# Performance work log

Hardware: AMD Instinct MI355X
Metric: run time of the kernel (lower is better)

Reference implementation:

```python
import jax, jax.numpy as jnp
import numpy as np

BZ, SEQ, IN_SZ, HID_SZ = 256, 512, 256, 256


def setup_inputs() -> dict:
    key = jax.random.key(0)
    k1, k2, k3, k4, k5 = jax.random.split(key, 5)
    stdv = 1.0 / np.sqrt(HID_SZ)
    return {
        "encoder_inputs": jax.random.normal(k1, (BZ, HID_SZ), dtype=jnp.float32),
        "decoder_inputs": jax.random.normal(k2, (BZ, SEQ, IN_SZ), dtype=jnp.float32),
        "U_i": jax.random.uniform(k3, (IN_SZ, HID_SZ), minval=-stdv, maxval=stdv, dtype=jnp.float32),
        "V_i": jax.random.uniform(k4, (HID_SZ, HID_SZ), minval=-stdv, maxval=stdv, dtype=jnp.float32),
        "b_i": jax.random.uniform(k5, (HID_SZ,), minval=-stdv, maxval=stdv, dtype=jnp.float32),
    }


def reference(encoder_inputs, decoder_inputs, U_i, V_i, b_i):
    # Sequential vanilla-RNN recurrence over time via lax.scan.
    # h_t = tanh(x_t @ U_i + h_{t-1} @ V_i + b_i)
    xs = jnp.swapaxes(decoder_inputs, 0, 1)  # [seq, bz, in]

    def step(h, x_t):
        h_new = jnp.tanh(x_t @ U_i + h @ V_i + b_i)
        return h_new, h_new

    _, outs = jax.lax.scan(step, encoder_inputs, xs)  # outs: [seq, bz, hid]
    decoder_outputs = jnp.swapaxes(outs, 0, 1)  # [bz, seq, hid]
    return (encoder_inputs, decoder_outputs)
```

## Files before the change

### kernel.cpp

```cpp
#include <hip/hip_runtime.h>
#include <hip/hip_bf16.h>


#define SEQn   512
#define HIDn   256
#define CHUNK  64
#define NCHUNK 8

typedef __attribute__((ext_vector_type(4))) float    floatx4;
typedef __attribute__((ext_vector_type(8))) _Float16 half8;

#define LDS_BARRIER() asm volatile("s_waitcnt lgkmcnt(0)\n\ts_barrier" ::: "memory")

__global__ __launch_bounds__(512, 1)
void rnn_fused(const float* __restrict__ enc, const float* __restrict__ x,
               const float* __restrict__ U,   const float* __restrict__ V,
               const float* __restrict__ bias, float* __restrict__ out)
{
    __shared__ _Float16 xbf[CHUNK][HIDn];
    __shared__ float    xu[CHUNK][HIDn + 1];
    __shared__ _Float16 hbuf[2][HIDn];

    const int tid = threadIdx.x;
    const int w   = tid >> 6;
    const int l   = tid & 63;
    const int lr  = l & 15;
    const int q   = l >> 4;
    const int b   = blockIdx.x;
    const int c0  = 32 * w + lr;

    half8 uf[2][8], vf[2][8];
    #pragma unroll
    for (int c = 0; c < 8; c++) {
        const float* up = U + (size_t)(32 * c + 8 * q) * HIDn + c0;
        const float* vp = V + (size_t)(32 * c + 8 * q) * HIDn + c0;
        #pragma unroll
        for (int nt = 0; nt < 2; nt++) {
            half8 tu, tv;
            #pragma unroll
            for (int j = 0; j < 8; j++) {
                tu[j] = (_Float16)up[(size_t)j * HIDn + 16 * nt];
                tv[j] = (_Float16)vp[(size_t)j * HIDn + 16 * nt];
            }
            uf[nt][c] = tu;
            vf[nt][c] = tv;
        }
    }

    const float b0 = bias[c0];
    const float b1 = bias[c0 + 16];

    if (tid < HIDn) {
        float h0 = enc[(size_t)b * HIDn + tid];
        out[(size_t)b * HIDn + tid] = h0;
        hbuf[0][tid] = (_Float16)h0;
    }

    const float* xb = x + (size_t)b * SEQn * HIDn;
    float* outDec   = out + (size_t)65536 + (size_t)b * SEQn * HIDn;

    const int srow = tid >> 3;
    const int scol = (tid & 7) * 32;

    const floatx4 zf = {0.f, 0.f, 0.f, 0.f};

    int p = 0;
    for (int g = 0; g < NCHUNK; g++) {
        const float* xs = xb + (size_t)(g * CHUNK + srow) * HIDn + scol;
        float4 xv[8];
        #pragma unroll
        for (int i = 0; i < 8; i++)
            xv[i] = *(const float4*)(xs + 4 * i);
        #pragma unroll
        for (int gi = 0; gi < 4; gi++) {
            half8 t;
            t[0] = (_Float16)xv[2*gi].x;   t[1] = (_Float16)xv[2*gi].y;
            t[2] = (_Float16)xv[2*gi].z;   t[3] = (_Float16)xv[2*gi].w;
            t[4] = (_Float16)xv[2*gi+1].x; t[5] = (_Float16)xv[2*gi+1].y;
            t[6] = (_Float16)xv[2*gi+1].z; t[7] = (_Float16)xv[2*gi+1].w;
            int grp = ((tid & 7) * 4 + gi) ^ (srow & 7);
            *(half8*)&xbf[srow][grp * 8] = t;
        }
        LDS_BARRIER();

        {
            floatx4 ga[2][4];
            #pragma unroll
            for (int c = 0; c < 8; c++) {
                half8 am[4];
                #pragma unroll
                for (int mt = 0; mt < 4; mt++) {
                    int row = 16 * mt + lr;
                    int grp = (4 * c + q) ^ (row & 7);
                    am[mt] = *(const half8*)&xbf[row][grp * 8];
                }
                #pragma unroll
                for (int mt = 0; mt < 4; mt++) {
                    ga[0][mt] = __builtin_amdgcn_mfma_f32_16x16x32_f16(
                        am[mt], uf[0][c], c ? ga[0][mt] : zf, 0, 0, 0);
                    ga[1][mt] = __builtin_amdgcn_mfma_f32_16x16x32_f16(
                        am[mt], uf[1][c], c ? ga[1][mt] : zf, 0, 0, 0);
                }
            }
            #pragma unroll
            for (int mt = 0; mt < 4; mt++)
                #pragma unroll
                for (int r = 0; r < 4; r++) {
                    int row = 16 * mt + 4 * q + r;
                    xu[row][c0]      = ga[0][mt][r] + b0;
                    xu[row][c0 + 16] = ga[1][mt][r] + b1;
                }
        }
        LDS_BARRIER();

        for (int tt = 0; tt < CHUNK; tt++) {
            half8 af[8];
            #pragma unroll
            for (int c = 0; c < 8; c++)
                af[c] = *(const half8*)&hbuf[p][32 * c + 8 * q];

            floatx4 acc[2][4];
            #pragma unroll
            for (int c = 0; c < 8; c++) {
                acc[0][c & 3] = __builtin_amdgcn_mfma_f32_16x16x32_f16(
                    af[c], vf[0][c], (c < 4) ? zf : acc[0][c & 3], 0, 0, 0);
                acc[1][c & 3] = __builtin_amdgcn_mfma_f32_16x16x32_f16(
                    af[c], vf[1][c], (c < 4) ? zf : acc[1][c & 3], 0, 0, 0);
            }

            float s0 = ((acc[0][0][0] + acc[0][1][0]) + (acc[0][2][0] + acc[0][3][0]))
                       + xu[tt][c0];
            float s1 = ((acc[1][0][0] + acc[1][1][0]) + (acc[1][2][0] + acc[1][3][0]))
                       + xu[tt][c0 + 16];
            float e0  = __expf(2.f * s0);
            float e1  = __expf(2.f * s1);
            float hv0 = 1.f - __fdividef(2.f, e0 + 1.f);
            float hv1 = 1.f - __fdividef(2.f, e1 + 1.f);

            if (q == 0) {
                hbuf[p ^ 1][c0]      = (_Float16)hv0;
                hbuf[p ^ 1][c0 + 16] = (_Float16)hv1;
                float* op = outDec + (size_t)(g * CHUNK + tt) * HIDn;
                op[c0]      = hv0;
                op[c0 + 16] = hv1;
            }
            p ^= 1;
            LDS_BARRIER();
        }
    }
}

extern "C" void kernel_launch(void* const* d_in, const int* in_sizes, int n_in,
                              void* d_out, int out_size, void* d_ws, size_t ws_size,
                              hipStream_t stream) {
    const float* enc  = (const float*)d_in[0];
    const float* x    = (const float*)d_in[1];
    const float* U    = (const float*)d_in[2];
    const float* V    = (const float*)d_in[3];
    const float* bias = (const float*)d_in[4];
    float* out = (float*)d_out;

    rnn_fused<<<256, 512, 0, stream>>>(enc, x, U, V, bias, out);
}
```

Before: 486.2 us.

## Halve block to four waves, each wave computing 64 hidden columns

The block shrinks from 8 waves to 4, and each wave now owns 64 hidden columns (four 16-wide MFMA tiles) instead of 32. In the recurrence, all 64 lanes now compute one tanh each and write the new h directly. Before, only the first quarter of each wave did this work. The aim is a cheaper per-timestep barrier and fuller lane use on the serial path. The cost is one wave per SIMD carrying twice the MFMA chain per step, with less latency hiding and higher register pressure from the doubled U/V fragments.

```diff
diff --git a/kernel.cpp b/kernel.cpp
--- a/kernel.cpp
+++ b/kernel.cpp
@@ -8,11 +8,12 @@
 #define NCHUNK 8
 
 typedef __attribute__((ext_vector_type(4))) float    floatx4;
+typedef __attribute__((ext_vector_type(4))) _Float16 half4;
 typedef __attribute__((ext_vector_type(8))) _Float16 half8;
 
 #define LDS_BARRIER() asm volatile("s_waitcnt lgkmcnt(0)\n\ts_barrier" ::: "memory")
 
-__global__ __launch_bounds__(512, 1)
+__global__ __launch_bounds__(256, 1)
 void rnn_fused(const float* __restrict__ enc, const float* __restrict__ x,
                const float* __restrict__ U,   const float* __restrict__ V,
                const float* __restrict__ bias, float* __restrict__ out)
@@ -27,15 +28,15 @@
     const int lr  = l & 15;
     const int q   = l >> 4;
     const int b   = blockIdx.x;
-    const int c0  = 32 * w + lr;
+    const int cw  = 64 * w;
 
-    half8 uf[2][8], vf[2][8];
+    half8 uf[4][8], vf[4][8];
     #pragma unroll
     for (int c = 0; c < 8; c++) {
-        const float* up = U + (size_t)(32 * c + 8 * q) * HIDn + c0;
-        const float* vp = V + (size_t)(32 * c + 8 * q) * HIDn + c0;
+        const float* up = U + (size_t)(32 * c + 8 * q) * HIDn + cw + lr;
+        const float* vp = V + (size_t)(32 * c + 8 * q) * HIDn + cw + lr;
         #pragma unroll
-        for (int nt = 0; nt < 2; nt++) {
+        for (int nt = 0; nt < 4; nt++) {
             half8 tu, tv;
             #pragma unroll
             for (int j = 0; j < 8; j++) {
@@ -47,10 +48,11 @@
         }
     }
 
-    const float b0 = bias[c0];
-    const float b1 = bias[c0 + 16];
+    float bv[4];
+    #pragma unroll
+    for (int nt = 0; nt < 4; nt++) bv[nt] = bias[cw + 16 * nt + lr];
 
-    if (tid < HIDn) {
+    {
         float h0 = enc[(size_t)b * HIDn + tid];
         out[(size_t)b * HIDn + tid] = h0;
         hbuf[0][tid] = (_Float16)h0;
@@ -59,32 +61,30 @@
     const float* xb = x + (size_t)b * SEQn * HIDn;
     float* outDec   = out + (size_t)65536 + (size_t)b * SEQn * HIDn;
 
-    const int srow = tid >> 3;
-    const int scol = (tid & 7) * 32;
+    const int srow = tid >> 2;
+    const int sc4  = tid & 3;
 
     const floatx4 zf = {0.f, 0.f, 0.f, 0.f};
 
     int p = 0;
     for (int g = 0; g < NCHUNK; g++) {
-        const float* xs = xb + (size_t)(g * CHUNK + srow) * HIDn + scol;
-        float4 xv[8];
+        const float* xs = xb + (size_t)(g * CHUNK + srow) * HIDn + 4 * sc4;
+        float4 xv[16];
         #pragma unroll
-        for (int i = 0; i < 8; i++)
-            xv[i] = *(const float4*)(xs + 4 * i);
+        for (int i = 0; i < 16; i++)
+            xv[i] = *(const float4*)(xs + 16 * i);
         #pragma unroll
-        for (int gi = 0; gi < 4; gi++) {
-            half8 t;
-            t[0] = (_Float16)xv[2*gi].x;   t[1] = (_Float16)xv[2*gi].y;
-            t[2] = (_Float16)xv[2*gi].z;   t[3] = (_Float16)xv[2*gi].w;
-            t[4] = (_Float16)xv[2*gi+1].x; t[5] = (_Float16)xv[2*gi+1].y;
-            t[6] = (_Float16)xv[2*gi+1].z; t[7] = (_Float16)xv[2*gi+1].w;
-            int grp = ((tid & 7) * 4 + gi) ^ (srow & 7);
-            *(half8*)&xbf[srow][grp * 8] = t;
+        for (int i = 0; i < 16; i++) {
+            half4 t;
+            t[0] = (_Float16)xv[i].x; t[1] = (_Float16)xv[i].y;
+            t[2] = (_Float16)xv[i].z; t[3] = (_Float16)xv[i].w;
+            int grp = (2 * i + (sc4 >> 1)) ^ (srow & 7);
+            *(half4*)&xbf[srow][grp * 8 + 4 * (sc4 & 1)] = t;
         }
         LDS_BARRIER();
 
         {
-            floatx4 ga[2][4];
+            floatx4 ga[4][4];
             #pragma unroll
             for (int c = 0; c < 8; c++) {
                 half8 am[4];
@@ -95,55 +95,54 @@
                     am[mt] = *(const half8*)&xbf[row][grp * 8];
                 }
                 #pragma unroll
-                for (int mt = 0; mt < 4; mt++) {
-                    ga[0][mt] = __builtin_amdgcn_mfma_f32_16x16x32_f16(
-                        am[mt], uf[0][c], c ? ga[0][mt] : zf, 0, 0, 0);
-                    ga[1][mt] = __builtin_amdgcn_mfma_f32_16x16x32_f16(
-                        am[mt], uf[1][c], c ? ga[1][mt] : zf, 0, 0, 0);
-                }
+                for (int mt = 0; mt < 4; mt++)
+                    #pragma unroll
+                    for (int nt = 0; nt < 4; nt++)
+                        ga[mt][nt] = __builtin_amdgcn_mfma_f32_16x16x32_f16(
+                            am[mt], uf[nt][c], c ? ga[mt][nt] : zf, 0, 0, 0);
             }
             #pragma unroll
             for (int mt = 0; mt < 4; mt++)
                 #pragma unroll
-                for (int r = 0; r < 4; r++) {
-                    int row = 16 * mt + 4 * q + r;
-                    xu[row][c0]      = ga[0][mt][r] + b0;
-                    xu[row][c0 + 16] = ga[1][mt][r] + b1;
-                }
+                for (int nt = 0; nt < 4; nt++)
+                    #pragma unroll
+                    for (int r = 0; r < 4; r++)
+                        xu[16 * mt + 4 * q + r][cw + 16 * nt + lr] =
+                            ga[mt][nt][r] + bv[nt];
         }
         LDS_BARRIER();
 
         for (int tt = 0; tt < CHUNK; tt++) {
+            float xuv = xu[tt][cw + l];
+
             half8 af[8];
             #pragma unroll
             for (int c = 0; c < 8; c++)
                 af[c] = *(const half8*)&hbuf[p][32 * c + 8 * q];
 
-            floatx4 acc[2][4];
+            floatx4 acc[4][2];
             #pragma unroll
             for (int c = 0; c < 8; c++) {
-                acc[0][c & 3] = __builtin_amdgcn_mfma_f32_16x16x32_f16(
-                    af[c], vf[0][c], (c < 4) ? zf : acc[0][c & 3], 0, 0, 0);
-                acc[1][c & 3] = __builtin_amdgcn_mfma_f32_16x16x32_f16(
-                    af[c], vf[1][c], (c < 4) ? zf : acc[1][c & 3], 0, 0, 0);
+                const int ch = c & 1;
+                #pragma unroll
+                for (int nt = 0; nt < 4; nt++)
+                    acc[nt][ch] = __builtin_amdgcn_mfma_f32_16x16x32_f16(
+                        af[c], vf[nt][c], (c < 2) ? zf : acc[nt][ch], 0, 0, 0);
             }
 
-            float s0 = ((acc[0][0][0] + acc[0][1][0]) + (acc[0][2][0] + acc[0][3][0]))
-                       + xu[tt][c0];
-            float s1 = ((acc[1][0][0] + acc[1][1][0]) + (acc[1][2][0] + acc[1][3][0]))
-                       + xu[tt][c0 + 16];
-            float e0  = __expf(2.f * s0);
-            float e1  = __expf(2.f * s1);
-            float hv0 = 1.f - __fdividef(2.f, e0 + 1.f);
-            float hv1 = 1.f - __fdividef(2.f, e1 + 1.f);
+            float a0 = acc[0][0][0] + acc[0][1][0];
+            float a1 = acc[1][0][0] + acc[1][1][0];
+            float a2 = acc[2][0][0] + acc[2][1][0];
+            float a3 = acc[3][0][0] + acc[3][1][0];
+            float t01 = (q & 1) ? a1 : a0;
+            float t23 = (q & 1) ? a3 : a2;
+            float s   = ((q & 2) ? t23 : t01) + xuv;
 
-            if (q == 0) {
-                hbuf[p ^ 1][c0]      = (_Float16)hv0;
-                hbuf[p ^ 1][c0 + 16] = (_Float16)hv1;
-                float* op = outDec + (size_t)(g * CHUNK + tt) * HIDn;
-                op[c0]      = hv0;
-                op[c0 + 16] = hv1;
-            }
+            float e  = __expf(2.f * s);
+            float hv = 1.f - __fdividef(2.f, e + 1.f);
+
+            hbuf[p ^ 1][cw + l] = (_Float16)hv;
+            outDec[(size_t)(g * CHUNK + tt) * HIDn + cw + l] = hv;
             p ^= 1;
             LDS_BARRIER();
         }
@@ -160,5 +159,5 @@
     const float* bias = (const float*)d_in[4];
     float* out = (float*)d_out;
 
-    rnn_fused<<<256, 512, 0, stream>>>(enc, x, U, V, bias, out);
+    rnn_fused<<<256, 256, 0, stream>>>(enc, x, U, V, bias, out);
 }
```

Measured after the change: 508.3 us. 1.05x slower.
